# Optimization experiments

Measured on AMD Instinct MI355X. Metric: run time of the kernel, lower is better.

Reference implementation:

```python
import jax, jax.numpy as jnp
import numpy as np

EMBED = 128
HEADS = 8
DEPTH = EMBED // HEADS
N, L = 32, 4096


def setup_inputs() -> dict:
    key = jax.random.key(0)
    ks = jax.random.split(key, 11)
    s = 1.0 / np.sqrt(EMBED)
    inp = {
        "values": jax.random.normal(ks[0], (N, L, EMBED), jnp.float32),
        "keys": jax.random.normal(ks[1], (N, L, EMBED), jnp.float32),
        "queries": jax.random.normal(ks[2], (N, L, EMBED), jnp.float32),
        "Wv": jax.random.normal(ks[3], (EMBED, EMBED), jnp.float32) * s,
        "bv": jnp.zeros((EMBED,), jnp.float32),
        "Wk": jax.random.normal(ks[4], (EMBED, EMBED), jnp.float32) * s,
        "bk": jnp.zeros((EMBED,), jnp.float32),
        "Wq": jax.random.normal(ks[5], (EMBED, EMBED), jnp.float32) * s,
        "bq": jnp.zeros((EMBED,), jnp.float32),
        "Wo": jax.random.normal(ks[6], (EMBED, EMBED), jnp.float32) * s,
        "bo": jnp.zeros((EMBED,), jnp.float32),
    }
    return inp


def reference(values, keys, queries, Wv, bv, Wk, bk, Wq, bq, Wo, bo):
    n, l, e = queries.shape
    h, d = HEADS, DEPTH
    # Linear projections (torch Linear: x @ W^T + b; here W stored as (in, out))
    v = (values @ Wv + bv).reshape(n, l, h, d)
    k = (keys @ Wk + bk).reshape(n, l, h, d)
    q = (queries @ Wq + bq).reshape(n, l, h, d)
    # Original einsum 'nbhd,mbhd->nhbm' attends across the BATCH axis at each
    # sequence position; the chunk loop over positions never mixes positions,
    # so it is equivalent to one vectorized einsum over all positions t.
    scores = jnp.einsum('nthd,mthd->nhtm', q, k)  # [N, H, L, N]
    attn = jax.nn.softmax(scores, axis=-1)
    out = jnp.einsum('nhtm,mthd->nthd', attn, v).reshape(n, l, e)
    return out @ Wo + bo
```

## Files before the change

### kernel.cpp

```cpp
#include <hip/hip_runtime.h>

#define LSEQ 4096

typedef __bf16 bf16x8 __attribute__((ext_vector_type(8)));
typedef float f32x16 __attribute__((ext_vector_type(16)));

union FU { unsigned u[4]; uint4 u4; bf16x8 v; };

__device__ __forceinline__ unsigned short bfb(float f) {
  __bf16 h = (__bf16)f;
  return __builtin_bit_cast(unsigned short, h);
}
__device__ __forceinline__ unsigned pk2(float a, float b) {
  return (unsigned)bfb(a) | ((unsigned)bfb(b) << 16);
}
__device__ __forceinline__ void xchg(unsigned P0, unsigned P1, unsigned P2, unsigned P3,
                                     const int hi, unsigned o[4]) {
  const unsigned sA = hi ? P0 : P2, sB = hi ? P1 : P3;
  const unsigned rA = __shfl_xor(sA, 32), rB = __shfl_xor(sB, 32);
  o[0] = hi ? rA : P0; o[1] = hi ? rB : P1;
  o[2] = hi ? P2 : rA; o[3] = hi ? P3 : rB;
}

__device__ __forceinline__ void loadW(const uint4* __restrict__ wf4, int mat, int nt,
                                      int l, FU w[9]) {
#pragma unroll
  for (int ks = 0; ks < 9; ++ks)
    w[ks].u4 = wf4[((mat * 4 + nt) * 9 + ks) * 64 + l];
}

__global__ __launch_bounds__(64) void repack(
    const float* __restrict__ Wv, const float* __restrict__ bv,
    const float* __restrict__ Wk, const float* __restrict__ bk,
    const float* __restrict__ Wq, const float* __restrict__ bq,
    const float* __restrict__ Wo, const float* __restrict__ bo,
    uint4* __restrict__ ws) {
  const int b = blockIdx.x;
  const int ks = b % 9, nt = (b / 9) & 3, m = b / 36;
  const float* Ws[4] = {Wv, Wk, Wq, Wo};
  const float* Bs[4] = {bv, bk, bq, bo};
  const int l = threadIdx.x, l31 = l & 31, hi = l >> 5;
  FU f;
  if (ks < 8) {
#pragma unroll
    for (int e = 0; e < 4; ++e) {
      const float a = Ws[m][(ks * 16 + hi * 8 + 2 * e) * 128 + nt * 32 + l31];
      const float c = Ws[m][(ks * 16 + hi * 8 + 2 * e + 1) * 128 + nt * 32 + l31];
      f.u[e] = pk2(a, c);
    }
  } else {
    f.u[0] = (hi == 0) ? (unsigned)bfb(Bs[m][nt * 32 + l31]) : 0u;
    f.u[1] = 0; f.u[2] = 0; f.u[3] = 0;
  }
  ws[b * 64 + l] = f.u4;
}

__global__ __launch_bounds__(256, 3) void fused_mha(
    const float* __restrict__ Xv, const float* __restrict__ Xk, const float* __restrict__ Xq,
    const uint4* __restrict__ wf4, float* __restrict__ out) {
  __shared__ uint4 xlds[3 * 8 * 64];
  __shared__ uint4 olds[8 * 64];
  const int tid = threadIdx.x;
  const int t = blockIdx.x;
  const int wid = tid >> 6, l = tid & 63;
  const int nt = wid, l31 = l & 31, hi = l >> 5;

  FU wfA[9], wfB[9];
  loadW(wf4, 0, nt, l, wfA);
  loadW(wf4, 1, nt, l, wfB);

  {
    const int r = tid >> 3, ksc = tid & 7;
    const float* Xs[3] = {Xv, Xk, Xq};
#pragma unroll
    for (int tau = 0; tau < 3; ++tau) {
      const float4* p4 = reinterpret_cast<const float4*>(
          Xs[tau] + ((long)r * LSEQ + t) * 128 + ksc * 16);
      const float4 a = p4[0], b = p4[1], c = p4[2], d = p4[3];
      FU lo, hb;
      lo.u[0] = pk2(a.x, a.y); lo.u[1] = pk2(a.z, a.w);
      lo.u[2] = pk2(b.x, b.y); lo.u[3] = pk2(b.z, b.w);
      hb.u[0] = pk2(c.x, c.y); hb.u[1] = pk2(c.z, c.w);
      hb.u[2] = pk2(d.x, d.y); hb.u[3] = pk2(d.z, d.w);
      xlds[(tau * 8 + ksc) * 64 + (r ^ ksc)] = lo.u4;
      xlds[(tau * 8 + ksc) * 64 + ((r ^ ksc) | 32)] = hb.u4;
    }
  }
  __syncthreads();

  FU cf;
  cf.u[0] = hi ? 0u : 0x00003F80u; cf.u[1] = 0; cf.u[2] = 0; cf.u[3] = 0;

  unsigned vpk[8];
  FU kf[2], qf[2];

  {
    f32x16 acc = {};
#pragma unroll
    for (int ks = 0; ks < 8; ++ks) {
      FU xf; xf.u4 = xlds[(0 * 8 + ks) * 64 + (l ^ ks)];
      acc = __builtin_amdgcn_mfma_f32_32x32x16_bf16(xf.v, wfA[ks].v, acc, 0, 0, 0);
    }
    acc = __builtin_amdgcn_mfma_f32_32x32x16_bf16(cf.v, wfA[8].v, acc, 0, 0, 0);
#pragma unroll
    for (int jv = 0; jv < 8; ++jv) vpk[jv] = pk2(acc[2 * jv], acc[2 * jv + 1]);
  }

  loadW(wf4, 2, nt, l, wfA);

  {
    f32x16 acc = {};
#pragma unroll
    for (int ks = 0; ks < 8; ++ks) {
      FU xf; xf.u4 = xlds[(1 * 8 + ks) * 64 + (l ^ ks)];
      acc = __builtin_amdgcn_mfma_f32_32x32x16_bf16(wfB[ks].v, xf.v, acc, 0, 0, 0);
    }
    acc = __builtin_amdgcn_mfma_f32_32x32x16_bf16(wfB[8].v, cf.v, acc, 0, 0, 0);
#pragma unroll
    for (int ch = 0; ch < 2; ++ch) {
      const int c8 = ch * 8;
      xchg(pk2(acc[c8 + 0], acc[c8 + 1]), pk2(acc[c8 + 2], acc[c8 + 3]),
           pk2(acc[c8 + 4], acc[c8 + 5]), pk2(acc[c8 + 6], acc[c8 + 7]), hi, kf[ch].u);
    }
  }

  loadW(wf4, 3, nt, l, wfB);

  {
    f32x16 acc = {};
#pragma unroll
    for (int ks = 0; ks < 8; ++ks) {
      FU xf; xf.u4 = xlds[(2 * 8 + ks) * 64 + (l ^ ks)];
      acc = __builtin_amdgcn_mfma_f32_32x32x16_bf16(wfA[ks].v, xf.v, acc, 0, 0, 0);
    }
    acc = __builtin_amdgcn_mfma_f32_32x32x16_bf16(wfA[8].v, cf.v, acc, 0, 0, 0);
#pragma unroll
    for (int ch = 0; ch < 2; ++ch) {
      const int c8 = ch * 8;
      xchg(pk2(acc[c8 + 0], acc[c8 + 1]), pk2(acc[c8 + 2], acc[c8 + 3]),
           pk2(acc[c8 + 4], acc[c8 + 5]), pk2(acc[c8 + 6], acc[c8 + 7]), hi, qf[ch].u);
    }
  }

  {
    FU vm0, vm1, vs0, vs1;
    xchg(vpk[0], vpk[1], vpk[2], vpk[3], hi, vm0.u);
    xchg(vpk[4], vpk[5], vpk[6], vpk[7], hi, vm1.u);
#pragma unroll
    for (int i = 0; i < 4; ++i) {
      vs0.u[i] = __shfl_xor(vm0.u[i], 16);
      vs1.u[i] = __shfl_xor(vm1.u[i], 16);
    }
#pragma unroll
    for (int ch = 0; ch < 2; ++ch) {
      const int h = nt * 2 + ch;
      const bool own = ((l31 >> 4) == ch);
      f32x16 zz = {};
      f32x16 S = __builtin_amdgcn_mfma_f32_32x32x16_bf16(kf[ch].v, qf[ch].v, zz, 0, 0, 0);
      float mx = S[0];
#pragma unroll
      for (int r = 1; r < 16; ++r) mx = fmaxf(mx, S[r]);
      mx = fmaxf(mx, __shfl_xor(mx, 32));
      float p[16], sum = 0.f;
#pragma unroll
      for (int r = 0; r < 16; ++r) {
        p[r] = exp2f((S[r] - mx) * 1.44269504089f);
        sum += p[r];
      }
      sum += __shfl_xor(sum, 32);
      const float inv = 1.0f / sum;
      FU pf0, pf1;
      xchg(pk2(p[0], p[1]), pk2(p[2], p[3]), pk2(p[4], p[5]), pk2(p[6], p[7]), hi, pf0.u);
      xchg(pk2(p[8], p[9]), pk2(p[10], p[11]), pk2(p[12], p[13]), pk2(p[14], p[15]), hi, pf1.u);
      FU v0, v1;
#pragma unroll
      for (int i = 0; i < 4; ++i) {
        v0.u[i] = own ? vm0.u[i] : vs0.u[i];
        v1.u[i] = own ? vm1.u[i] : vs1.u[i];
      }
      f32x16 z2 = {};
      f32x16 Ot = __builtin_amdgcn_mfma_f32_32x32x16_bf16(v0.v, pf0.v, z2, 0, 0, 0);
      Ot = __builtin_amdgcn_mfma_f32_32x32x16_bf16(v1.v, pf1.v, Ot, 0, 0, 0);
      FU ofr;
      xchg(pk2(Ot[0] * inv, Ot[1] * inv), pk2(Ot[2] * inv, Ot[3] * inv),
           pk2(Ot[4] * inv, Ot[5] * inv), pk2(Ot[6] * inv, Ot[7] * inv), hi, ofr.u);
      olds[h * 64 + l] = ofr.u4;
    }
  }
  __syncthreads();

  {
    f32x16 acc = {};
#pragma unroll
    for (int h = 0; h < 8; ++h) {
      FU of; of.u4 = olds[h * 64 + l];
      acc = __builtin_amdgcn_mfma_f32_32x32x16_bf16(of.v, wfB[h].v, acc, 0, 0, 0);
    }
    acc = __builtin_amdgcn_mfma_f32_32x32x16_bf16(cf.v, wfB[8].v, acc, 0, 0, 0);
#pragma unroll
    for (int r = 0; r < 16; ++r) {
      const int n = (r & 3) + ((r >> 2) << 3) + (hi << 2);
      out[((long)n * LSEQ + t) * 128 + nt * 32 + l31] = acc[r];
    }
  }
}

extern "C" void kernel_launch(void* const* d_in, const int* in_sizes, int n_in,
                              void* d_out, int out_size, void* d_ws, size_t ws_size,
                              hipStream_t stream) {
  const float* values  = (const float*)d_in[0];
  const float* keys    = (const float*)d_in[1];
  const float* queries = (const float*)d_in[2];
  const float* Wv = (const float*)d_in[3];
  const float* bv = (const float*)d_in[4];
  const float* Wk = (const float*)d_in[5];
  const float* bk = (const float*)d_in[6];
  const float* Wq = (const float*)d_in[7];
  const float* bq = (const float*)d_in[8];
  const float* Wo = (const float*)d_in[9];
  const float* bo = (const float*)d_in[10];

  repack<<<dim3(144), dim3(64), 0, stream>>>(Wv, bv, Wk, bk, Wq, bq, Wo, bo,
                                             (uint4*)d_ws);
  fused_mha<<<dim3(LSEQ), dim3(256), 0, stream>>>(
      values, keys, queries, (const uint4*)d_ws, (float*)d_out);
}
```

Measured before the change: 65.67 us.

## Software-pipeline weight loads with inline asm and explicit vmcnt waits

```diff
diff --git a/kernel.cpp b/kernel.cpp
--- a/kernel.cpp
+++ b/kernel.cpp
@@ -4,8 +4,10 @@
 
 typedef __bf16 bf16x8 __attribute__((ext_vector_type(8)));
 typedef float f32x16 __attribute__((ext_vector_type(16)));
-
-union FU { unsigned u[4]; uint4 u4; bf16x8 v; };
+typedef unsigned u32x4 __attribute__((ext_vector_type(4)));
+
+union FU { unsigned u[4]; u32x4 uv; bf16x8 v; };
+union FX { u32x4 uv; float f[4]; };
 
 __device__ __forceinline__ unsigned short bfb(float f) {
   __bf16 h = (__bf16)f;
@@ -22,19 +24,28 @@
   o[2] = hi ? P2 : rA; o[3] = hi ? P3 : rB;
 }
 
-__device__ __forceinline__ void loadW(const uint4* __restrict__ wf4, int mat, int nt,
-                                      int l, FU w[9]) {
-#pragma unroll
-  for (int ks = 0; ks < 9; ++ks)
-    w[ks].u4 = wf4[((mat * 4 + nt) * 9 + ks) * 64 + l];
-}
+__device__ __forceinline__ u32x4 gload(const void* p) {
+  u32x4 d;
+  asm volatile("global_load_dwordx4 %0, %1, off" : "=v"(d) : "v"(p));
+  return d;
+}
+#define WAITV(n)                                              \
+  do {                                                        \
+    asm volatile("s_waitcnt vmcnt(" #n ")" ::: "memory");     \
+    __builtin_amdgcn_sched_barrier(0);                        \
+  } while (0)
+#define WAITL                                                 \
+  do {                                                        \
+    asm volatile("s_waitcnt lgkmcnt(0)" ::: "memory");        \
+    __builtin_amdgcn_sched_barrier(0);                        \
+  } while (0)
 
 __global__ __launch_bounds__(64) void repack(
     const float* __restrict__ Wv, const float* __restrict__ bv,
     const float* __restrict__ Wk, const float* __restrict__ bk,
     const float* __restrict__ Wq, const float* __restrict__ bq,
     const float* __restrict__ Wo, const float* __restrict__ bo,
-    uint4* __restrict__ ws) {
+    u32x4* __restrict__ ws) {
   const int b = blockIdx.x;
   const int ks = b % 9, nt = (b / 9) & 3, m = b / 36;
   const float* Ws[4] = {Wv, Wk, Wq, Wo};
@@ -52,41 +63,62 @@
     f.u[0] = (hi == 0) ? (unsigned)bfb(Bs[m][nt * 32 + l31]) : 0u;
     f.u[1] = 0; f.u[2] = 0; f.u[3] = 0;
   }
-  ws[b * 64 + l] = f.u4;
+  ws[b * 64 + l] = f.uv;
 }
 
 __global__ __launch_bounds__(256, 3) void fused_mha(
     const float* __restrict__ Xv, const float* __restrict__ Xk, const float* __restrict__ Xq,
-    const uint4* __restrict__ wf4, float* __restrict__ out) {
-  __shared__ uint4 xlds[3 * 8 * 64];
-  __shared__ uint4 olds[8 * 64];
+    const u32x4* __restrict__ wf4, float* __restrict__ out) {
+  __shared__ u32x4 xlds[3 * 8 * 64];
+  __shared__ u32x4 olds[8 * 64];
   const int tid = threadIdx.x;
   const int t = blockIdx.x;
   const int wid = tid >> 6, l = tid & 63;
   const int nt = wid, l31 = l & 31, hi = l >> 5;
 
-  FU wfA[9], wfB[9];
-  loadW(wf4, 0, nt, l, wfA);
-  loadW(wf4, 1, nt, l, wfB);
-
+  u32x4 xr[12];
   {
     const int r = tid >> 3, ksc = tid & 7;
     const float* Xs[3] = {Xv, Xk, Xq};
 #pragma unroll
     for (int tau = 0; tau < 3; ++tau) {
-      const float4* p4 = reinterpret_cast<const float4*>(
-          Xs[tau] + ((long)r * LSEQ + t) * 128 + ksc * 16);
-      const float4 a = p4[0], b = p4[1], c = p4[2], d = p4[3];
+      const float* bp = Xs[tau] + ((long)r * LSEQ + t) * 128 + ksc * 16;
+#pragma unroll
+      for (int i = 0; i < 4; ++i) xr[tau * 4 + i] = gload(bp + i * 4);
+    }
+  }
+  FU wfA[9], wfB[9], wfC[9], wfD[9];
+  {
+    const u32x4* wb = wf4 + ((0 * 4 + nt) * 9) * 64 + l;
+#pragma unroll
+    for (int ks = 0; ks < 9; ++ks) wfA[ks].uv = gload(wb + ks * 64);
+  }
+
+  WAITV(9);
+  {
+    const int r = tid >> 3, ksc = tid & 7;
+#pragma unroll
+    for (int tau = 0; tau < 3; ++tau) {
+      FX a, b, c, d;
+      a.uv = xr[tau * 4 + 0]; b.uv = xr[tau * 4 + 1];
+      c.uv = xr[tau * 4 + 2]; d.uv = xr[tau * 4 + 3];
       FU lo, hb;
-      lo.u[0] = pk2(a.x, a.y); lo.u[1] = pk2(a.z, a.w);
-      lo.u[2] = pk2(b.x, b.y); lo.u[3] = pk2(b.z, b.w);
-      hb.u[0] = pk2(c.x, c.y); hb.u[1] = pk2(c.z, c.w);
-      hb.u[2] = pk2(d.x, d.y); hb.u[3] = pk2(d.z, d.w);
-      xlds[(tau * 8 + ksc) * 64 + (r ^ ksc)] = lo.u4;
-      xlds[(tau * 8 + ksc) * 64 + ((r ^ ksc) | 32)] = hb.u4;
-    }
-  }
-  __syncthreads();
+      lo.u[0] = pk2(a.f[0], a.f[1]); lo.u[1] = pk2(a.f[2], a.f[3]);
+      lo.u[2] = pk2(b.f[0], b.f[1]); lo.u[3] = pk2(b.f[2], b.f[3]);
+      hb.u[0] = pk2(c.f[0], c.f[1]); hb.u[1] = pk2(c.f[2], c.f[3]);
+      hb.u[2] = pk2(d.f[0], d.f[1]); hb.u[3] = pk2(d.f[2], d.f[3]);
+      xlds[(tau * 8 + ksc) * 64 + (r ^ ksc)] = lo.uv;
+      xlds[(tau * 8 + ksc) * 64 + ((r ^ ksc) | 32)] = hb.uv;
+    }
+  }
+  WAITL;
+  __builtin_amdgcn_s_barrier();
+
+  {
+    const u32x4* wb = wf4 + ((1 * 4 + nt) * 9) * 64 + l;
+#pragma unroll
+    for (int ks = 0; ks < 9; ++ks) wfB[ks].uv = gload(wb + ks * 64);
+  }
 
   FU cf;
   cf.u[0] = hi ? 0u : 0x00003F80u; cf.u[1] = 0; cf.u[2] = 0; cf.u[3] = 0;
@@ -94,11 +126,12 @@
   unsigned vpk[8];
   FU kf[2], qf[2];
 
+  WAITV(9);
   {
     f32x16 acc = {};
 #pragma unroll
     for (int ks = 0; ks < 8; ++ks) {
-      FU xf; xf.u4 = xlds[(0 * 8 + ks) * 64 + (l ^ ks)];
+      FU xf; xf.uv = xlds[(0 * 8 + ks) * 64 + (l ^ ks)];
       acc = __builtin_amdgcn_mfma_f32_32x32x16_bf16(xf.v, wfA[ks].v, acc, 0, 0, 0);
     }
     acc = __builtin_amdgcn_mfma_f32_32x32x16_bf16(cf.v, wfA[8].v, acc, 0, 0, 0);
@@ -106,13 +139,18 @@
     for (int jv = 0; jv < 8; ++jv) vpk[jv] = pk2(acc[2 * jv], acc[2 * jv + 1]);
   }
 
-  loadW(wf4, 2, nt, l, wfA);
-
+  {
+    const u32x4* wb = wf4 + ((2 * 4 + nt) * 9) * 64 + l;
+#pragma unroll
+    for (int ks = 0; ks < 9; ++ks) wfC[ks].uv = gload(wb + ks * 64);
+  }
+
+  WAITV(9);
   {
     f32x16 acc = {};
 #pragma unroll
     for (int ks = 0; ks < 8; ++ks) {
-      FU xf; xf.u4 = xlds[(1 * 8 + ks) * 64 + (l ^ ks)];
+      FU xf; xf.uv = xlds[(1 * 8 + ks) * 64 + (l ^ ks)];
       acc = __builtin_amdgcn_mfma_f32_32x32x16_bf16(wfB[ks].v, xf.v, acc, 0, 0, 0);
     }
     acc = __builtin_amdgcn_mfma_f32_32x32x16_bf16(wfB[8].v, cf.v, acc, 0, 0, 0);
@@ -124,16 +162,21 @@
     }
   }
 
-  loadW(wf4, 3, nt, l, wfB);
-
+  {
+    const u32x4* wb = wf4 + ((3 * 4 + nt) * 9) * 64 + l;
+#pragma unroll
+    for (int ks = 0; ks < 9; ++ks) wfD[ks].uv = gload(wb + ks * 64);
+  }
+
+  WAITV(9);
   {
     f32x16 acc = {};
 #pragma unroll
     for (int ks = 0; ks < 8; ++ks) {
-      FU xf; xf.u4 = xlds[(2 * 8 + ks) * 64 + (l ^ ks)];
-      acc = __builtin_amdgcn_mfma_f32_32x32x16_bf16(wfA[ks].v, xf.v, acc, 0, 0, 0);
-    }
-    acc = __builtin_amdgcn_mfma_f32_32x32x16_bf16(wfA[8].v, cf.v, acc, 0, 0, 0);
+      FU xf; xf.uv = xlds[(2 * 8 + ks) * 64 + (l ^ ks)];
+      acc = __builtin_amdgcn_mfma_f32_32x32x16_bf16(wfC[ks].v, xf.v, acc, 0, 0, 0);
+    }
+    acc = __builtin_amdgcn_mfma_f32_32x32x16_bf16(wfC[8].v, cf.v, acc, 0, 0, 0);
 #pragma unroll
     for (int ch = 0; ch < 2; ++ch) {
       const int c8 = ch * 8;
@@ -184,19 +227,21 @@
       FU ofr;
       xchg(pk2(Ot[0] * inv, Ot[1] * inv), pk2(Ot[2] * inv, Ot[3] * inv),
            pk2(Ot[4] * inv, Ot[5] * inv), pk2(Ot[6] * inv, Ot[7] * inv), hi, ofr.u);
-      olds[h * 64 + l] = ofr.u4;
-    }
-  }
-  __syncthreads();
-
+      olds[h * 64 + l] = ofr.uv;
+    }
+  }
+  WAITL;
+  __builtin_amdgcn_s_barrier();
+
+  WAITV(0);
   {
     f32x16 acc = {};
 #pragma unroll
     for (int h = 0; h < 8; ++h) {
-      FU of; of.u4 = olds[h * 64 + l];
-      acc = __builtin_amdgcn_mfma_f32_32x32x16_bf16(of.v, wfB[h].v, acc, 0, 0, 0);
-    }
-    acc = __builtin_amdgcn_mfma_f32_32x32x16_bf16(cf.v, wfB[8].v, acc, 0, 0, 0);
+      FU of; of.uv = olds[h * 64 + l];
+      acc = __builtin_amdgcn_mfma_f32_32x32x16_bf16(of.v, wfD[h].v, acc, 0, 0, 0);
+    }
+    acc = __builtin_amdgcn_mfma_f32_32x32x16_bf16(cf.v, wfD[8].v, acc, 0, 0, 0);
 #pragma unroll
     for (int r = 0; r < 16; ++r) {
       const int n = (r & 3) + ((r >> 2) << 3) + (hi << 2);
@@ -221,7 +266,7 @@
   const float* bo = (const float*)d_in[10];
 
   repack<<<dim3(144), dim3(64), 0, stream>>>(Wv, bv, Wk, bk, Wq, bq, Wo, bo,
-                                             (uint4*)d_ws);
+                                             (u32x4*)d_ws);
   fused_mha<<<dim3(LSEQ), dim3(256), 0, stream>>>(
-      values, keys, queries, (const uint4*)d_ws, (float*)d_out);
-}
+      values, keys, queries, (const u32x4*)d_ws, (float*)d_out);
+}
```

Measured after the change: 66.46 us. Within noise of the previous version (+1.2%).
